# Optimization experiments

Measured on AMD Instinct MI355X. Metric: run time of the kernel, lower is better.

## Reference

```python
import jax, jax.numpy as jnp
import numpy as np

H, W = 384, 384          # render resolution (init h, w)
TH, TW = 1024, 1024      # texture resolution
N, V, F = 2, 2048, 2048  # batch, vertices/texcoords, faces
CHUNK = 32               # faces per rasterization scan step
EPS = 1e-8


def setup_inputs() -> dict:
    key = jax.random.key(0)
    k = jax.random.split(key, 5)
    # vertices in front of camera, z ~ 3
    v = jax.random.normal(k[0], (N, V, 3), jnp.float32) * jnp.array([0.5, 0.5, 0.3], jnp.float32) + jnp.array([0.0, 0.0, 3.0], jnp.float32)
    tex = jax.random.uniform(k[1], (N, 3, TH, TW), jnp.float32)
    campos = jnp.zeros((N, 3), jnp.float32)
    camrot = jnp.broadcast_to(jnp.eye(3, dtype=jnp.float32), (N, 3, 3))
    focal = jnp.broadcast_to(400.0 * jnp.eye(2, dtype=jnp.float32), (N, 2, 2))
    princpt = jnp.broadcast_to(jnp.array([W / 2.0, H / 2.0], jnp.float32), (N, 2))
    vt = jax.random.uniform(k[2], (V, 2), jnp.float32)
    vt = vt.at[:, 1].set(1.0 - vt[:, 1])  # flip_uvs=True applied at init
    vi = jax.random.randint(k[3], (F, 3), 0, V, jnp.int32)
    vti = jax.random.randint(k[4], (F, 3), 0, V, jnp.int32)
    return {"v": v, "tex": tex, "campos": campos, "camrot": camrot, "focal": focal, "princpt": princpt, "vt": vt, "vi": vi, "vti": vti}


def _bary(x0, y0, x1, y1, x2, y2, px, py):
    # signed-area-normalized screen-space barycentrics (both windings accepted)
    area = (x1 - x0) * (y2 - y0) - (y1 - y0) * (x2 - x0)
    ok = jnp.abs(area) > 1e-9
    inv = 1.0 / jnp.where(ok, area, 1.0)
    b0 = ((x2 - x1) * (py - y1) - (y2 - y1) * (px - x1)) * inv
    b1 = ((x0 - x2) * (py - y2) - (y0 - y2) * (px - x2)) * inv
    b2 = ((x1 - x0) * (py - y0) - (y1 - y0) * (px - x0)) * inv
    return b0, b1, b2, ok


def _rasterize_one(v_pix, vi):
    # z-buffered rasterization via scan over face chunks; pixel centers at +0.5
    px = jnp.arange(W, dtype=jnp.float32)[None, None, :] + 0.5
    py = jnp.arange(H, dtype=jnp.float32)[None, :, None] + 0.5
    nch = F // CHUNK
    fids = jnp.arange(F, dtype=jnp.int32).reshape(nch, CHUNK)
    vic = vi.reshape(nch, CHUNK, 3)

    def body(carry, inp):
        zbuf, ibuf = carry
        fid, f = inp
        tri = v_pix[f]                       # [CHUNK,3,3]
        x = tri[:, :, 0][:, :, None, None]
        y = tri[:, :, 1][:, :, None, None]
        z = tri[:, :, 2][:, :, None, None]
        b0, b1, b2, ok = _bary(x[:, 0], y[:, 0], x[:, 1], y[:, 1], x[:, 2], y[:, 2], px, py)
        inside = (b0 >= 0) & (b1 >= 0) & (b2 >= 0) & ok
        zinv = b0 / z[:, 0] + b1 / z[:, 1] + b2 / z[:, 2]  # perspective-correct 1/depth
        d = jnp.where(inside & (zinv > EPS), 1.0 / jnp.maximum(zinv, EPS), jnp.inf)
        amin = jnp.argmin(d, axis=0)
        dmin = jnp.min(d, axis=0)
        upd = dmin < zbuf
        return (jnp.where(upd, dmin, zbuf), jnp.where(upd, fid[amin], ibuf)), None

    init = (jnp.full((H, W), jnp.inf, jnp.float32), jnp.full((H, W), -1, jnp.int32))
    (_, ib), _ = jax.lax.scan(body, init, (fids, vic))
    return ib


def _render_one(v_pix, vi, idx):
    # recompute perspective-correct barycentrics / depth for winning faces (differentiable)
    px = jnp.arange(W, dtype=jnp.float32)[None, :] + 0.5
    py = jnp.arange(H, dtype=jnp.float32)[:, None] + 0.5
    tri = v_pix[vi[jnp.maximum(idx, 0)]]     # [H,W,3,3]
    x, y, z = tri[..., 0], tri[..., 1], tri[..., 2]
    b0, b1, b2, ok = _bary(x[..., 0], y[..., 0], x[..., 1], y[..., 1], x[..., 2], y[..., 2], px, py)
    w0, w1, w2 = b0 / z[..., 0], b1 / z[..., 1], b2 / z[..., 2]
    zinv = jnp.maximum(w0 + w1 + w2, EPS)
    mask = idx >= 0
    depth = jnp.where(mask, 1.0 / zinv, 0.0)
    bary = jnp.where(mask[None], jnp.stack([w0, w1, w2], 0) / zinv[None], 0.0)  # [3,H,W]
    return depth, bary


def _interp_one(attr, fvi, idx, bary):
    vals = attr[fvi[jnp.maximum(idx, 0)]]    # [H,W,3,C]
    return jnp.einsum('hwkc,khw->chw', vals, bary)


def _grid_sample_one(tex, grid):
    # bilinear, align_corners=False, padding_mode='border'
    ix = ((grid[..., 0] + 1.0) * TW - 1.0) * 0.5
    iy = ((grid[..., 1] + 1.0) * TH - 1.0) * 0.5
    ix0 = jnp.floor(ix); iy0 = jnp.floor(iy)
    wx = ix - ix0; wy = iy - iy0
    x0 = jnp.clip(ix0.astype(jnp.int32), 0, TW - 1)
    x1 = jnp.clip(ix0.astype(jnp.int32) + 1, 0, TW - 1)
    y0 = jnp.clip(iy0.astype(jnp.int32), 0, TH - 1)
    y1 = jnp.clip(iy0.astype(jnp.int32) + 1, 0, TH - 1)
    g = lambda yi, xi: tex[:, yi, xi]        # [C,H,W]
    return (g(y0, x0) * (1 - wx) * (1 - wy) + g(y0, x1) * wx * (1 - wy)
            + g(y1, x0) * (1 - wx) * wy + g(y1, x1) * wx * wy)


_rasterize = jax.vmap(_rasterize_one, (0, None))
_render = jax.vmap(_render_one, (0, None, 0))
_interp = jax.vmap(_interp_one, (0, None, 0, 0))
_grid_sample = jax.vmap(_grid_sample_one)


def reference(v, tex, campos, camrot, focal, princpt, vt, vi, vti):
    # camera transform: v_cam = R (v - campos); v_pix = focal @ (xy/z) + princpt, z preserved
    v_cam = jnp.einsum('nij,nvj->nvi', camrot, v - campos[:, None, :])
    z = v_cam[..., 2:3]
    xy = jnp.einsum('nij,nvj->nvi', focal, v_cam[..., :2] / z) + princpt[:, None, :]
    v_pix = jnp.concatenate([xy, z], axis=-1)
    idx = _rasterize(jax.lax.stop_gradient(v_pix), vi)   # rasterize under no_grad
    mask = idx >= 0
    depth_img, bary_img = _render(v_pix, vi, idx)
    uv = jnp.broadcast_to(2.0 * vt - 1.0, (v.shape[0], vt.shape[0], 2))
    vt_img = _interp(uv, vti, idx, bary_img).transpose(0, 2, 3, 1)  # NHWC uv grid
    image = _grid_sample(tex, vt_img) * mask[:, None].astype(tex.dtype)
    return image
```

## Files before the change

kernel.cpp:

```cpp
#include <hip/hip_runtime.h>
#include <math.h>

#pragma clang fp contract(off)

#define NN 2
#define VV 2048
#define FF 2048
#define HH 384
#define WW 384
#define TH 1024
#define TW 1024
#define EPSD 1e-08
#define SLICES 4
#define FPS (FF / SLICES)
#define SETUP_BLOCKS ((NN * FF + 255) / 256)
#define CLEAR_BLOCKS ((NN * HH * WW + 255) / 256)

__device__ __forceinline__ float mulr(float a, float b) {
    float p = a * b;
    asm("" : "+v"(p));
    return p;
}


__global__ __launch_bounds__(256) void setup_and_clear(
    const float* __restrict__ v, const float* __restrict__ campos,
    const float* __restrict__ camrot, const float* __restrict__ focal,
    const float* __restrict__ princpt, const int* __restrict__ vi,
    const float* __restrict__ vt, const int* __restrict__ vti,
    double* __restrict__ dface, double* __restrict__ uvface,
    float4* __restrict__ cull, unsigned long long* __restrict__ keybuf)
{
#pragma clang fp contract(off)
    if (blockIdx.x >= SETUP_BLOCKS) {
        int idx = (blockIdx.x - SETUP_BLOCKS) * 256 + threadIdx.x;
        if (idx < NN * HH * WW) keybuf[idx] = 0ull;
        return;
    }
    int t = blockIdx.x * blockDim.x + threadIdx.x;
    if (t >= NN * FF) return;
    int n = t / FF, f = t % FF;
    const float* cr = camrot + n * 9;
    const float* cp = campos + n * 3;
    const float* fo = focal + n * 4;
    const float* pp = princpt + n * 2;
    float X[3], Y[3], Z[3];
    for (int k = 0; k < 3; ++k) {
        int vid = vi[f * 3 + k];
        const float* vp = v + ((size_t)n * VV + vid) * 3;
        float d0 = vp[0] - cp[0];
        float d1 = vp[1] - cp[1];
        float d2 = vp[2] - cp[2];
        float c0 = (mulr(cr[0], d0) + mulr(cr[1], d1)) + mulr(cr[2], d2);
        float c1 = (mulr(cr[3], d0) + mulr(cr[4], d1)) + mulr(cr[5], d2);
        float c2 = (mulr(cr[6], d0) + mulr(cr[7], d1)) + mulr(cr[8], d2);
        float u = c0 / c2;
        float w = c1 / c2;
        X[k] = (mulr(fo[0], u) + mulr(fo[1], w)) + pp[0];
        Y[k] = (mulr(fo[2], u) + mulr(fo[3], w)) + pp[1];
        Z[k] = c2;
    }
    float area = mulr(X[1] - X[0], Y[2] - Y[0]) - mulr(Y[1] - Y[0], X[2] - X[0]);
    bool ok = fabsf(area) > 1e-9f;
    float inv = ok ? (1.0f / area) : __builtin_nanf("");
    float e0x = X[2] - X[1], e0y = Y[2] - Y[1];
    float e1x = X[0] - X[2], e1y = Y[0] - Y[2];
    float e2x = X[1] - X[0], e2y = Y[1] - Y[0];
    double invd = (double)inv;
    double e0xd = (double)e0x, e0yd = (double)e0y;
    double e1xd = (double)e1x, e1yd = (double)e1y;
    double e2xd = (double)e2x, e2yd = (double)e2y;
    double x0d = (double)X[0], y0d = (double)Y[0];
    double x1d = (double)X[1], y1d = (double)Y[1];
    double x2d = (double)X[2], y2d = (double)Y[2];
    double rz0 = 1.0 / (double)Z[0];
    double rz1 = 1.0 / (double)Z[1];
    double rz2 = 1.0 / (double)Z[2];
    double Gx0 = -e0yd * invd, Gy0 = e0xd * invd, Gc0 = (e0yd * x1d - e0xd * y1d) * invd;
    double Gx1 = -e1yd * invd, Gy1 = e1xd * invd, Gc1 = (e1yd * x2d - e1xd * y2d) * invd;
    double Gx2 = -e2yd * invd, Gy2 = e2xd * invd, Gc2 = (e2yd * x0d - e2xd * y0d) * invd;
    double Zx = Gx0 * rz0 + Gx1 * rz1 + Gx2 * rz2;
    double Zy = Gy0 * rz0 + Gy1 * rz1 + Gy2 * rz2;
    double Zc = Gc0 * rz0 + Gc1 * rz1 + Gc2 * rz2;
    double* dd = dface + (size_t)t * 16;
    dd[0] = Gx0; dd[1] = Gy0; dd[2] = Gc0;
    dd[3] = Gx1; dd[4] = Gy1; dd[5] = Gc1;
    dd[6] = Gx2; dd[7] = Gy2; dd[8] = Gc2;
    dd[9] = Zx; dd[10] = Zy; dd[11] = Zc;
    dd[12] = 0.0; dd[13] = 0.0; dd[14] = 0.0; dd[15] = 0.0;
    int i0 = vti[f * 3 + 0], i1 = vti[f * 3 + 1], i2 = vti[f * 3 + 2];
    double u0d = (double)(2.0f * vt[i0 * 2 + 0] - 1.0f), v0d = (double)(2.0f * vt[i0 * 2 + 1] - 1.0f);
    double u1d = (double)(2.0f * vt[i1 * 2 + 0] - 1.0f), v1d = (double)(2.0f * vt[i1 * 2 + 1] - 1.0f);
    double u2d = (double)(2.0f * vt[i2 * 2 + 0] - 1.0f), v2d = (double)(2.0f * vt[i2 * 2 + 1] - 1.0f);
    double W0x = Gx0 * rz0, W0y = Gy0 * rz0, W0c = Gc0 * rz0;
    double W1x = Gx1 * rz1, W1y = Gy1 * rz1, W1c = Gc1 * rz1;
    double W2x = Gx2 * rz2, W2y = Gy2 * rz2, W2c = Gc2 * rz2;
    double* uv = uvface + (size_t)t * 8;
    uv[0] = (u0d * W0x + u1d * W1x) + u2d * W2x;
    uv[1] = (u0d * W0y + u1d * W1y) + u2d * W2y;
    uv[2] = (u0d * W0c + u1d * W1c) + u2d * W2c;
    uv[3] = (v0d * W0x + v1d * W1x) + v2d * W2x;
    uv[4] = (v0d * W0y + v1d * W1y) + v2d * W2y;
    uv[5] = (v0d * W0c + v1d * W1c) + v2d * W2c;
    uv[6] = 0.0; uv[7] = 0.0;
    float s = (area > 0.0f) ? 1.0f : -1.0f;
    float A0 = -e0y * s, B0 = e0x * s;
    float C0 = s * (float)(e0yd * x1d - e0xd * y1d);
    float A1 = -e1y * s, B1 = e1x * s;
    float C1 = s * (float)(e1yd * x2d - e1xd * y2d);
    float A2 = -e2y * s, B2 = e2x * s;
    float C2 = s * (float)(e2yd * x0d - e2xd * y0d);
    if (!ok) { C0 = -3e30f; C1 = -3e30f; C2 = -3e30f; }
    float xmn = fminf(fminf(X[0], X[1]), X[2]);
    float xmx = fmaxf(fmaxf(X[0], X[1]), X[2]);
    float ymn = fminf(fminf(Y[0], Y[1]), Y[2]);
    float ymx = fmaxf(fmaxf(Y[0], Y[1]), Y[2]);
    float4* cu = cull + (size_t)t * 4;
    cu[0] = make_float4(xmn, ymn, xmx, ymx);
    cu[1] = make_float4(A0, B0, C0, A1);
    cu[2] = make_float4(B1, C1, A2, B2);
    cu[3] = make_float4(C2, 0.0f, 0.0f, 0.0f);
}

__device__ __forceinline__ bool edge_keep(float A, float B, float C,
                                          float xlo, float xhi, float ylo, float yhi) {
    float m = A * ((A > 0.0f) ? xhi : xlo) + B * ((B > 0.0f) ? yhi : ylo) + C;
    return m >= -1.0f;
}

__global__ __launch_bounds__(256) void raster(
    const double* __restrict__ dface, const float4* __restrict__ cull,
    unsigned long long* __restrict__ keybuf)
{
#pragma clang fp contract(fast)
    __shared__ int s_cnt[4];
    __shared__ int s_list[4][FPS];
    int nz = blockIdx.z;
    int n = nz / SLICES, slice = nz % SLICES;
    int tx0 = blockIdx.x * 16, ty0 = blockIdx.y * 16;
    int tid = threadIdx.x;
    int lane = tid & 63;
    int wv = tid >> 6;
    if (tid < 4) s_cnt[tid] = 0;
    __syncthreads();
    float xlo = (float)tx0, ylo = (float)ty0;
    for (int j = tid; j < FPS; j += 256) {
        int f = slice + j * SLICES;
        const float4* cu = cull + ((size_t)n * FF + f) * 4;
        float4 bb = cu[0];
        if (bb.x <= xlo + 16.0f && bb.z >= xlo && bb.y <= ylo + 16.0f && bb.w >= ylo) {
            float4 c1 = cu[1], c2 = cu[2], c3 = cu[3];
            #pragma unroll
            for (int q = 0; q < 4; ++q) {
                float qxlo = xlo + (float)((q & 1) * 8), qxhi = qxlo + 8.0f;
                float qylo = ylo + (float)((q >> 1) * 8), qyhi = qylo + 8.0f;
                if (bb.x <= qxhi && bb.z >= qxlo && bb.y <= qyhi && bb.w >= qylo &&
                    edge_keep(c1.x, c1.y, c1.z, qxlo, qxhi, qylo, qyhi) &&
                    edge_keep(c1.w, c2.x, c2.y, qxlo, qxhi, qylo, qyhi) &&
                    edge_keep(c2.z, c2.w, c3.x, qxlo, qxhi, qylo, qyhi)) {
                    int p = atomicAdd(&s_cnt[q], 1);
                    s_list[q][p] = f;
                }
            }
        }
    }
    __syncthreads();
    int cnt = s_cnt[wv];
    int qx0 = tx0 + (wv & 1) * 8;
    int qy0 = ty0 + (wv >> 1) * 8;
    double px = (double)(qx0 + (lane & 7)) + 0.5;
    double py = (double)(qy0 + (lane >> 3)) + 0.5;
    unsigned long long best = 0ull;
    const double* gbase = dface + (size_t)n * FF * 16;
    for (int i = 0; i < cnt; ++i) {
        int fid = __builtin_amdgcn_readfirstlane(s_list[wv][i]);
        const double* g = gbase + (size_t)fid * 16;
        double zinv = g[9] * px + (g[10] * py + g[11]);
        unsigned long long key =
            ((unsigned long long)__double_as_longlong(zinv) & ~0x7FFull)
            | (unsigned long long)(2047 - fid);
        bool cand = (zinv > EPSD) && (key > best);
        if (__any(cand)) {
            double b0 = g[0] * px + (g[1] * py + g[2]);
            double b1 = g[3] * px + (g[4] * py + g[5]);
            double b2 = g[6] * px + (g[7] * py + g[8]);
            if (cand && fmin(fmin(b0, b1), b2) >= 0.0) best = key;
        }
    }
    if (best) {
        int x = qx0 + (lane & 7), y = qy0 + (lane >> 3);
        atomicMax(keybuf + ((size_t)n * HH + y) * WW + x, best);
    }
}

__global__ __launch_bounds__(256) void render(
    const double* __restrict__ dface, const double* __restrict__ uvface,
    const unsigned long long* __restrict__ keybuf,
    const float* __restrict__ tex, float* __restrict__ out)
{
    int t = blockIdx.x * blockDim.x + threadIdx.x;
    if (t >= NN * HH * WW) return;
    int n = t / (HH * WW);
    int p = t % (HH * WW);
    int y = p / WW, x = p % WW;
    unsigned long long k = keybuf[t];
    int f = k ? (2047 - (int)(k & 0x7FFull)) : -1;
    size_t o0 = ((size_t)(n * 3 + 0) * HH + y) * WW + x;
    size_t o1 = ((size_t)(n * 3 + 1) * HH + y) * WW + x;
    size_t o2 = ((size_t)(n * 3 + 2) * HH + y) * WW + x;
    if (f < 0) {
        out[o0] = 0.0f; out[o1] = 0.0f; out[o2] = 0.0f;
        return;
    }
    const double* g = dface + ((size_t)n * FF + f) * 16;
    const double* uv = uvface + ((size_t)n * FF + f) * 8;
    double px = (double)x + 0.5, py = (double)y + 0.5;
    double s = g[9] * px + (g[10] * py + g[11]);
    double zq = fmax(s, EPSD);
    double rzq = 1.0 / zq;
    double gx = (uv[0] * px + (uv[1] * py + uv[2])) * rzq;
    double gy = (uv[3] * px + (uv[4] * py + uv[5])) * rzq;
    double ix = ((gx + 1.0) * (double)TW - 1.0) * 0.5;
    double iy = ((gy + 1.0) * (double)TH - 1.0) * 0.5;
    double fx0 = floor(ix), fy0 = floor(iy);
    double wx = ix - fx0, wy = iy - fy0;
    int x0 = min(max((int)fx0, 0), TW - 1);
    int x1 = min(max((int)fx0 + 1, 0), TW - 1);
    int y0 = min(max((int)fy0, 0), TH - 1);
    int y1 = min(max((int)fy0 + 1, 0), TH - 1);
    double omwx = 1.0 - wx, omwy = 1.0 - wy;
    bool pair = (x1 == x0 + 1);
    #pragma unroll
    for (int c = 0; c < 3; ++c) {
        const float* tc = tex + ((size_t)n * 3 + c) * TH * TW;
        float g00, g01, g10, g11;
        if (pair) {
            float2 r0 = *(const float2*)(tc + (size_t)y0 * TW + x0);
            float2 r1 = *(const float2*)(tc + (size_t)y1 * TW + x0);
            g00 = r0.x; g01 = r0.y; g10 = r1.x; g11 = r1.y;
        } else {
            g00 = tc[(size_t)y0 * TW + x0];
            g01 = tc[(size_t)y0 * TW + x1];
            g10 = tc[(size_t)y1 * TW + x0];
            g11 = tc[(size_t)y1 * TW + x1];
        }
        double val = ((((double)g00 * omwx) * omwy + ((double)g01 * wx) * omwy)
                      + ((double)g10 * omwx) * wy) + ((double)g11 * wx) * wy;
        size_t oo = (c == 0) ? o0 : ((c == 1) ? o1 : o2);
        out[oo] = (float)val;
    }
}

extern "C" void kernel_launch(void* const* d_in, const int* in_sizes, int n_in,
                              void* d_out, int out_size, void* d_ws, size_t ws_size,
                              hipStream_t stream) {
    const float* v = (const float*)d_in[0];
    const float* tex = (const float*)d_in[1];
    const float* campos = (const float*)d_in[2];
    const float* camrot = (const float*)d_in[3];
    const float* focal = (const float*)d_in[4];
    const float* princpt = (const float*)d_in[5];
    const float* vt = (const float*)d_in[6];
    const int* vi = (const int*)d_in[7];
    const int* vti = (const int*)d_in[8];
    float* out = (float*)d_out;

    char* ws = (char*)d_ws;
    double* dface = (double*)ws;
    double* uvface = (double*)(ws + 524288);
    float4* cull = (float4*)(ws + 524288 + 262144);
    unsigned long long* keybuf =
        (unsigned long long*)(ws + 524288 + 262144 + 262144);

    setup_and_clear<<<dim3(SETUP_BLOCKS + CLEAR_BLOCKS), dim3(256), 0, stream>>>(
        v, campos, camrot, focal, princpt, vi, vt, vti, dface, uvface, cull, keybuf);
    raster<<<dim3(WW / 16, HH / 16, NN * SLICES), dim3(256), 0, stream>>>(
        dface, cull, keybuf);
    render<<<dim3((NN * HH * WW + 255) / 256), dim3(256), 0, stream>>>(
        dface, uvface, keybuf, tex, out);
}
```

Before: 156.5 us.

## Sort faces front-to-back by max inverse depth and early-exit raster loop

Adds a per-batch bitonic sort kernel that orders faces by an upper bound on inverse depth and writes a strided permutation across slices. Per-quad binning now uses a wave ballot instead of shared atomics, and the per-pixel loop exits once every lane's best key beats the next face's bound. Slices are raised from 4 to 16 for more parallelism. This adds an extra launch and a single-block-per-batch sort, which is serial overhead.

Measured after the change: 234.0 us. 49.6% more time.

```diff
diff --git a/kernel.cpp b/kernel.cpp
--- a/kernel.cpp
+++ b/kernel.cpp
@@ -11,7 +11,7 @@
 #define TH 1024
 #define TW 1024
 #define EPSD 1e-08
-#define SLICES 4
+#define SLICES 16
 #define FPS (FF / SLICES)
 #define SETUP_BLOCKS ((NN * FF + 255) / 256)
 #define CLEAR_BLOCKS ((NN * HH * WW + 255) / 256)
@@ -87,7 +87,10 @@
     dd[3] = Gx1; dd[4] = Gy1; dd[5] = Gc1;
     dd[6] = Gx2; dd[7] = Gy2; dd[8] = Gc2;
     dd[9] = Zx; dd[10] = Zy; dd[11] = Zc;
-    dd[12] = 0.0; dd[13] = 0.0; dd[14] = 0.0; dd[15] = 0.0;
+    double ubz = fmax(fmax(rz0, rz1), rz2);
+    ((unsigned long long*)dd)[12] =
+        ((unsigned long long)__double_as_longlong(ubz) & ~0x7FFull) | 2047ull;
+    dd[13] = 0.0; dd[14] = 0.0; dd[15] = 0.0;
     int i0 = vti[f * 3 + 0], i1 = vti[f * 3 + 1], i2 = vti[f * 3 + 2];
     double u0d = (double)(2.0f * vt[i0 * 2 + 0] - 1.0f), v0d = (double)(2.0f * vt[i0 * 2 + 1] - 1.0f);
     double u1d = (double)(2.0f * vt[i1 * 2 + 0] - 1.0f), v1d = (double)(2.0f * vt[i1 * 2 + 1] - 1.0f);
@@ -122,6 +125,36 @@
     cu[3] = make_float4(C2, 0.0f, 0.0f, 0.0f);
 }
 
+__global__ __launch_bounds__(256) void order(
+    const double* __restrict__ dface, unsigned short* __restrict__ perm)
+{
+    __shared__ unsigned long long sk[FF];
+    int n = blockIdx.x, tid = threadIdx.x;
+    for (int i = tid; i < FF; i += 256) {
+        unsigned long long k =
+            ((const unsigned long long*)dface)[((size_t)(n * FF + i)) * 16 + 12];
+        sk[i] = (k & ~0x7FFull) | (unsigned long long)i;
+    }
+    __syncthreads();
+    for (int k = 2; k <= FF; k <<= 1) {
+        for (int j = k >> 1; j > 0; j >>= 1) {
+            for (int i = tid; i < FF; i += 256) {
+                int ixj = i ^ j;
+                if (ixj > i) {
+                    unsigned long long a = sk[i], b = sk[ixj];
+                    bool up = ((i & k) == 0);
+                    if (up ? (a < b) : (a > b)) { sk[i] = b; sk[ixj] = a; }
+                }
+            }
+            __syncthreads();
+        }
+    }
+    for (int i = tid; i < FF; i += 256) {
+        unsigned short fid = (unsigned short)(sk[i] & 0x7FFull);
+        perm[((size_t)n * SLICES + (i % SLICES)) * FPS + (i / SLICES)] = fid;
+    }
+}
+
 __device__ __forceinline__ bool edge_keep(float A, float B, float C,
                                           float xlo, float xhi, float ylo, float yhi) {
     float m = A * ((A > 0.0f) ? xhi : xlo) + B * ((B > 0.0f) ? yhi : ylo) + C;
@@ -130,10 +163,10 @@
 
 __global__ __launch_bounds__(256) void raster(
     const double* __restrict__ dface, const float4* __restrict__ cull,
+    const unsigned short* __restrict__ perm,
     unsigned long long* __restrict__ keybuf)
 {
 #pragma clang fp contract(fast)
-    __shared__ int s_cnt[4];
     __shared__ int s_list[4][FPS];
     int nz = blockIdx.z;
     int n = nz / SLICES, slice = nz % SLICES;
@@ -141,33 +174,29 @@
     int tid = threadIdx.x;
     int lane = tid & 63;
     int wv = tid >> 6;
-    if (tid < 4) s_cnt[tid] = 0;
-    __syncthreads();
-    float xlo = (float)tx0, ylo = (float)ty0;
-    for (int j = tid; j < FPS; j += 256) {
-        int f = slice + j * SLICES;
-        const float4* cu = cull + ((size_t)n * FF + f) * 4;
-        float4 bb = cu[0];
-        if (bb.x <= xlo + 16.0f && bb.z >= xlo && bb.y <= ylo + 16.0f && bb.w >= ylo) {
-            float4 c1 = cu[1], c2 = cu[2], c3 = cu[3];
-            #pragma unroll
-            for (int q = 0; q < 4; ++q) {
-                float qxlo = xlo + (float)((q & 1) * 8), qxhi = qxlo + 8.0f;
-                float qylo = ylo + (float)((q >> 1) * 8), qyhi = qylo + 8.0f;
-                if (bb.x <= qxhi && bb.z >= qxlo && bb.y <= qyhi && bb.w >= qylo &&
-                    edge_keep(c1.x, c1.y, c1.z, qxlo, qxhi, qylo, qyhi) &&
-                    edge_keep(c1.w, c2.x, c2.y, qxlo, qxhi, qylo, qyhi) &&
-                    edge_keep(c2.z, c2.w, c3.x, qxlo, qxhi, qylo, qyhi)) {
-                    int p = atomicAdd(&s_cnt[q], 1);
-                    s_list[q][p] = f;
-                }
-            }
-        }
-    }
-    __syncthreads();
-    int cnt = s_cnt[wv];
     int qx0 = tx0 + (wv & 1) * 8;
     int qy0 = ty0 + (wv >> 1) * 8;
+    float qxlo = (float)qx0, qxhi = qxlo + 8.0f;
+    float qylo = (float)qy0, qyhi = qylo + 8.0f;
+    const unsigned short* pm = perm + ((size_t)n * SLICES + slice) * FPS;
+    int cnt = 0;
+    #pragma unroll
+    for (int r2 = 0; r2 < FPS / 64; ++r2) {
+        int fid = (int)pm[r2 * 64 + lane];
+        const float4* cu = cull + ((size_t)n * FF + fid) * 4;
+        float4 bb = cu[0];
+        bool keep = false;
+        if (bb.x <= qxhi && bb.z >= qxlo && bb.y <= qyhi && bb.w >= qylo) {
+            float4 c1 = cu[1], c2 = cu[2], c3 = cu[3];
+            keep = edge_keep(c1.x, c1.y, c1.z, qxlo, qxhi, qylo, qyhi) &&
+                   edge_keep(c1.w, c2.x, c2.y, qxlo, qxhi, qylo, qyhi) &&
+                   edge_keep(c2.z, c2.w, c3.x, qxlo, qxhi, qylo, qyhi);
+        }
+        unsigned long long mask = __ballot(keep);
+        int pos = cnt + (int)__popcll(mask & ((1ull << lane) - 1ull));
+        if (keep) s_list[wv][pos] = fid;
+        cnt += (int)__popcll(mask);
+    }
     double px = (double)(qx0 + (lane & 7)) + 0.5;
     double py = (double)(qy0 + (lane >> 3)) + 0.5;
     unsigned long long best = 0ull;
@@ -175,6 +204,8 @@
     for (int i = 0; i < cnt; ++i) {
         int fid = __builtin_amdgcn_readfirstlane(s_list[wv][i]);
         const double* g = gbase + (size_t)fid * 16;
+        unsigned long long ub = ((const unsigned long long*)g)[12];
+        if (__all(best >= ub)) break;
         double zinv = g[9] * px + (g[10] * py + g[11]);
         unsigned long long key =
             ((unsigned long long)__double_as_longlong(zinv) & ~0x7FFull)
@@ -271,11 +302,13 @@
     float4* cull = (float4*)(ws + 524288 + 262144);
     unsigned long long* keybuf =
         (unsigned long long*)(ws + 524288 + 262144 + 262144);
+    unsigned short* perm = (unsigned short*)(ws + 3407872);
 
     setup_and_clear<<<dim3(SETUP_BLOCKS + CLEAR_BLOCKS), dim3(256), 0, stream>>>(
         v, campos, camrot, focal, princpt, vi, vt, vti, dface, uvface, cull, keybuf);
+    order<<<dim3(NN), dim3(256), 0, stream>>>(dface, perm);
     raster<<<dim3(WW / 16, HH / 16, NN * SLICES), dim3(256), 0, stream>>>(
-        dface, cull, keybuf);
+        dface, cull, perm, keybuf);
     render<<<dim3((NN * HH * WW + 255) / 256), dim3(256), 0, stream>>>(
         dface, uvface, keybuf, tex, out);
 }
```
